# Performance work log

Measured on AMD Instinct MI355X. Metric: run time of the kernel, lower is better.

## Reference

```python
import jax, jax.numpy as jnp
import numpy as np

B, D_IN, D_OUT = 8192, 1024, 1024


def setup_inputs() -> dict:
    key = jax.random.key(0)
    k1, k2 = jax.random.split(key)
    x = jax.random.normal(k1, (B, D_IN), dtype=jnp.float32)
    # Keras add_weight(shape=(3, input_dim, output_dim), initializer='uniform')
    kernel = jax.random.normal(k2, (3, D_IN, D_OUT), dtype=jnp.float32) * 0.05
    return {"x": x, "kernel": kernel}


def reference(x, kernel):
    # x: (B, D). Layer does expand_dims(axis=1) -> (B, 1, D) (seq_len == 1).
    output_dim = kernel.shape[-1]
    xe = x[:, None, :]                                   # (B, 1, D)
    q = jnp.einsum('bsd,do->bso', xe, kernel[0])         # (B, 1, O)
    k = jnp.einsum('bsd,do->bso', xe, kernel[1])         # (B, 1, O)
    v = jnp.einsum('bsd,do->bso', xe, kernel[2])         # (B, 1, O)
    scores = jnp.einsum('bqo,bko->bqk', q, k) / jnp.sqrt(
        jnp.asarray(output_dim, x.dtype))                # (B, 1, 1)
    attn = jax.nn.softmax(scores, axis=-1)
    out = jnp.einsum('bqk,bko->bqo', attn, v)            # (B, 1, O)
    return out
```

## Files before the change

kernel.cpp:

```cpp
#include <hip/hip_runtime.h>
#include <hip/hip_bf16.h>
#include <stdint.h>

#define AS1 __attribute__((address_space(1)))
#define AS3 __attribute__((address_space(3)))

typedef __attribute__((ext_vector_type(8))) short bf16x8_t;
typedef __attribute__((ext_vector_type(4))) float f32x4_t;

#define DDIM 1024
#define BM 128
#define BN 128
#define BK 32

static __device__ inline ushort f32_to_bf16_rne(float f) {
  union { float f; uint32_t u; } v;
  v.f = f;
  v.u += 0x7FFFu + ((v.u >> 16) & 1u);
  return (ushort)(v.u >> 16);
}

__global__ __launch_bounds__(256) void transpose_w(const float* __restrict__ W,
                                                   ushort* __restrict__ Wt) {
  __shared__ float tile[64][65];
  const int t  = threadIdx.x;
  const int bk = blockIdx.x;
  const int bn = blockIdx.y;
#pragma unroll
  for (int s = 0; s < 4; ++s) {
    const int slot = (s << 8) + t;
    const int r    = slot >> 4;
    const int c4   = (slot & 15) << 2;
    const float4 v = *(const float4*)(W + (size_t)(bk * 64 + r) * DDIM + bn * 64 + c4);
    tile[r][c4 + 0] = v.x; tile[r][c4 + 1] = v.y;
    tile[r][c4 + 2] = v.z; tile[r][c4 + 3] = v.w;
  }
  __syncthreads();
#pragma unroll
  for (int s = 0; s < 2; ++s) {
    const int slot = (s << 8) + t;
    const int n    = slot >> 3;
    const int k8   = (slot & 7) << 3;
    union { ushort h[8]; uint4 u; } tmp;
#pragma unroll
    for (int j = 0; j < 8; ++j) tmp.h[j] = f32_to_bf16_rne(tile[k8 + j][n]);
    *(uint4*)(Wt + (size_t)(bn * 64 + n) * DDIM + bk * 64 + k8) = tmp.u;
  }
}

__global__ __launch_bounds__(256) void gemm_xw(const float* __restrict__ X,
                                               const ushort* __restrict__ Wt,
                                               float* __restrict__ C) {
  __shared__ __align__(16) ushort As[BM * BK];
  __shared__ __align__(16) ushort Bs[BN * BK];

  const int t    = threadIdx.x;
  const int wave = t >> 6;
  const int lane = t & 63;
  const int m0 = blockIdx.x * BM;
  const int n0 = blockIdx.y * BN;

  const int srow  = (wave << 4) + (lane >> 2);
  const int skcol = (lane & 3) << 3;
  const ushort* bptr0 = Wt + (size_t)(n0 + srow) * DDIM + skcol;
  const ushort* bptr1 = Wt + (size_t)(n0 + 64 + srow) * DDIM + skcol;

  const int ar = t >> 2;
  const int ak = (t & 3) << 3;
  const float* aptr0 = X + (size_t)(m0 + ar) * DDIM + ak;
  const float* aptr1 = X + (size_t)(m0 + 64 + ar) * DDIM + ak;
  ushort* asw0 = &As[(ar << 5) + ak];
  ushort* asw1 = &As[((ar + 64) << 5) + ak];

  const int wr = (wave >> 1) << 6;
  const int wc = (wave & 1) << 6;
  const int fr = lane & 15;
  const int fq = lane >> 4;

  f32x4_t acc[4][4] = {};

  AS3 char* ldsB = (AS3 char*)Bs;
  const int woff = wave << 10;

  for (int kt = 0; kt < DDIM; kt += BK) {
    const float4 a00 = *(const float4*)(aptr0);
    const float4 a01 = *(const float4*)(aptr0 + 4);
    const float4 a10 = *(const float4*)(aptr1);
    const float4 a11 = *(const float4*)(aptr1 + 4);
    aptr0 += BK; aptr1 += BK;

    __syncthreads();

    __builtin_amdgcn_global_load_lds((const AS1 void*)bptr0, (AS3 void*)(ldsB + woff),        16, 0, 0);
    __builtin_amdgcn_global_load_lds((const AS1 void*)bptr1, (AS3 void*)(ldsB + 4096 + woff), 16, 0, 0);
    bptr0 += BK; bptr1 += BK;

    union { ushort h[8]; bf16x8_t v; } c0, c1;
    c0.h[0] = f32_to_bf16_rne(a00.x); c0.h[1] = f32_to_bf16_rne(a00.y);
    c0.h[2] = f32_to_bf16_rne(a00.z); c0.h[3] = f32_to_bf16_rne(a00.w);
    c0.h[4] = f32_to_bf16_rne(a01.x); c0.h[5] = f32_to_bf16_rne(a01.y);
    c0.h[6] = f32_to_bf16_rne(a01.z); c0.h[7] = f32_to_bf16_rne(a01.w);
    c1.h[0] = f32_to_bf16_rne(a10.x); c1.h[1] = f32_to_bf16_rne(a10.y);
    c1.h[2] = f32_to_bf16_rne(a10.z); c1.h[3] = f32_to_bf16_rne(a10.w);
    c1.h[4] = f32_to_bf16_rne(a11.x); c1.h[5] = f32_to_bf16_rne(a11.y);
    c1.h[6] = f32_to_bf16_rne(a11.z); c1.h[7] = f32_to_bf16_rne(a11.w);
    *(bf16x8_t*)asw0 = c0.v;
    *(bf16x8_t*)asw1 = c1.v;

    __syncthreads();

    bf16x8_t af[4], bfr[4];
#pragma unroll
    for (int mi = 0; mi < 4; ++mi)
      af[mi] = *(const bf16x8_t*)&As[((wr + (mi << 4) + fr) << 5) + (fq << 3)];
#pragma unroll
    for (int ni = 0; ni < 4; ++ni)
      bfr[ni] = *(const bf16x8_t*)&Bs[((wc + (ni << 4) + fr) << 5) + (fq << 3)];
#pragma unroll
    for (int mi = 0; mi < 4; ++mi)
#pragma unroll
      for (int ni = 0; ni < 4; ++ni)
        acc[mi][ni] = __builtin_amdgcn_mfma_f32_16x16x32_bf16(af[mi], bfr[ni], acc[mi][ni], 0, 0, 0);
  }

#pragma unroll
  for (int mi = 0; mi < 4; ++mi) {
#pragma unroll
    for (int r = 0; r < 4; ++r) {
      const int row = m0 + wr + (mi << 4) + (fq << 2) + r;
      float* crow = C + (size_t)row * DDIM + n0 + wc + fr;
#pragma unroll
      for (int ni = 0; ni < 4; ++ni)
        crow[ni << 4] = acc[mi][ni][r];
    }
  }
}

extern "C" void kernel_launch(void* const* d_in, const int* in_sizes, int n_in,
                              void* d_out, int out_size, void* d_ws, size_t ws_size,
                              hipStream_t stream) {
  const float* x    = (const float*)d_in[0];
  const float* kern = (const float*)d_in[1];
  const float* W = kern + (size_t)2 * DDIM * DDIM;
  ushort* Wt = (ushort*)d_ws;
  const int M = in_sizes[0] / DDIM;

  transpose_w<<<dim3(DDIM / 64, DDIM / 64), 256, 0, stream>>>(W, Wt);
  gemm_xw<<<dim3(M / BM, DDIM / BN), 256, 0, stream>>>(x, Wt, (float*)d_out);
}
```

Before: 130.7 us.

## Pre-convert X to bf16 and use smaller-tile swizzled all-DMA GEMM

Adds a separate kernel that converts X to bf16 in workspace, then runs a new GEMM that loads both A and B tiles straight into LDS with global_load_lds. It uses a 64x128 tile with launch bounds for higher occupancy and an XOR swizzle to avoid LDS bank conflicts. This removes the per-iteration fp32 load and convert from the GEMM main loop. In exchange it adds an extra pass over X (read fp32, write bf16, reread) and one more launch, and falls back to the old path if the workspace is too small.

```diff
diff --git a/kernel.cpp b/kernel.cpp
--- a/kernel.cpp
+++ b/kernel.cpp
@@ -9,9 +9,8 @@
 typedef __attribute__((ext_vector_type(4))) float f32x4_t;
 
 #define DDIM 1024
-#define BM 128
-#define BN 128
-#define BK 32
+#define WT_ELEMS ((size_t)DDIM * DDIM)
+#define XB_ELEMS ((size_t)8192 * DDIM)
 
 static __device__ inline ushort f32_to_bf16_rne(float f) {
   union { float f; uint32_t u; } v;
@@ -48,53 +47,125 @@
   }
 }
 
+__global__ __launch_bounds__(256) void convert_x(const float* __restrict__ X,
+                                                 ushort* __restrict__ Xb) {
+  const size_t i = ((size_t)blockIdx.x * 256 + threadIdx.x) << 3;
+  const float4 v0 = *(const float4*)(X + i);
+  const float4 v1 = *(const float4*)(X + i + 4);
+  union { ushort h[8]; uint4 u; } o;
+  o.h[0] = f32_to_bf16_rne(v0.x); o.h[1] = f32_to_bf16_rne(v0.y);
+  o.h[2] = f32_to_bf16_rne(v0.z); o.h[3] = f32_to_bf16_rne(v0.w);
+  o.h[4] = f32_to_bf16_rne(v1.x); o.h[5] = f32_to_bf16_rne(v1.y);
+  o.h[6] = f32_to_bf16_rne(v1.z); o.h[7] = f32_to_bf16_rne(v1.w);
+  *(uint4*)(Xb + i) = o.u;
+}
+
+__global__ __launch_bounds__(256, 4) void gemm_bb(const ushort* __restrict__ Xb,
+                                                  const ushort* __restrict__ Wt,
+                                                  float* __restrict__ C) {
+  __shared__ __align__(16) ushort As[64 * 32];
+  __shared__ __align__(16) ushort Bs[128 * 32];
+
+  const int t    = threadIdx.x;
+  const int wave = t >> 6;
+  const int lane = t & 63;
+  const int m0 = blockIdx.x * 64;
+  const int n0 = blockIdx.y * 128;
+
+  const int s  = (wave << 6) + lane;
+  const int sr = s >> 2;
+  const int sc = (s & 3) ^ ((sr >> 1) & 3);
+  const ushort* aptr  = Xb + (size_t)(m0 + sr) * DDIM + (sc << 3);
+  const ushort* bptr0 = Wt + (size_t)(n0 + sr) * DDIM + (sc << 3);
+  const ushort* bptr1 = Wt + (size_t)(n0 + 64 + sr) * DDIM + (sc << 3);
+
+  AS3 char* ldsA = (AS3 char*)As;
+  AS3 char* ldsB = (AS3 char*)Bs;
+  const int woff = wave << 10;
+
+  const int wr = (wave >> 1) << 5;
+  const int wc = (wave & 1) << 6;
+  const int fr = lane & 15;
+  const int fq = lane >> 4;
+
+  f32x4_t acc[2][4] = {};
+
+  for (int kt = 0; kt < DDIM; kt += 32) {
+    __syncthreads();
+    __builtin_amdgcn_global_load_lds((const AS1 void*)aptr,  (AS3 void*)(ldsA + woff),        16, 0, 0);
+    __builtin_amdgcn_global_load_lds((const AS1 void*)bptr0, (AS3 void*)(ldsB + woff),        16, 0, 0);
+    __builtin_amdgcn_global_load_lds((const AS1 void*)bptr1, (AS3 void*)(ldsB + 4096 + woff), 16, 0, 0);
+    aptr += 32; bptr0 += 32; bptr1 += 32;
+    __syncthreads();
+
+    bf16x8_t af[2], bfr[4];
+#pragma unroll
+    for (int mi = 0; mi < 2; ++mi) {
+      const int r = wr + (mi << 4) + fr;
+      af[mi] = *(const bf16x8_t*)&As[(r << 5) + ((fq ^ ((r >> 1) & 3)) << 3)];
+    }
+#pragma unroll
+    for (int ni = 0; ni < 4; ++ni) {
+      const int r = wc + (ni << 4) + fr;
+      bfr[ni] = *(const bf16x8_t*)&Bs[(r << 5) + ((fq ^ ((r >> 1) & 3)) << 3)];
+    }
+#pragma unroll
+    for (int mi = 0; mi < 2; ++mi)
+#pragma unroll
+      for (int ni = 0; ni < 4; ++ni)
+        acc[mi][ni] = __builtin_amdgcn_mfma_f32_16x16x32_bf16(af[mi], bfr[ni], acc[mi][ni], 0, 0, 0);
+  }
+
+#pragma unroll
+  for (int mi = 0; mi < 2; ++mi) {
+#pragma unroll
+    for (int r = 0; r < 4; ++r) {
+      const int row = m0 + wr + (mi << 4) + (fq << 2) + r;
+      float* crow = C + (size_t)row * DDIM + n0 + wc + fr;
+#pragma unroll
+      for (int ni = 0; ni < 4; ++ni)
+        crow[ni << 4] = acc[mi][ni][r];
+    }
+  }
+}
+
 __global__ __launch_bounds__(256) void gemm_xw(const float* __restrict__ X,
                                                const ushort* __restrict__ Wt,
                                                float* __restrict__ C) {
-  __shared__ __align__(16) ushort As[BM * BK];
-  __shared__ __align__(16) ushort Bs[BN * BK];
-
+  __shared__ __align__(16) ushort As[128 * 32];
+  __shared__ __align__(16) ushort Bs[128 * 32];
   const int t    = threadIdx.x;
   const int wave = t >> 6;
   const int lane = t & 63;
-  const int m0 = blockIdx.x * BM;
-  const int n0 = blockIdx.y * BN;
-
+  const int m0 = blockIdx.x * 128;
+  const int n0 = blockIdx.y * 128;
   const int srow  = (wave << 4) + (lane >> 2);
   const int skcol = (lane & 3) << 3;
   const ushort* bptr0 = Wt + (size_t)(n0 + srow) * DDIM + skcol;
   const ushort* bptr1 = Wt + (size_t)(n0 + 64 + srow) * DDIM + skcol;
-
   const int ar = t >> 2;
   const int ak = (t & 3) << 3;
   const float* aptr0 = X + (size_t)(m0 + ar) * DDIM + ak;
   const float* aptr1 = X + (size_t)(m0 + 64 + ar) * DDIM + ak;
   ushort* asw0 = &As[(ar << 5) + ak];
   ushort* asw1 = &As[((ar + 64) << 5) + ak];
-
   const int wr = (wave >> 1) << 6;
   const int wc = (wave & 1) << 6;
   const int fr = lane & 15;
   const int fq = lane >> 4;
-
   f32x4_t acc[4][4] = {};
-
   AS3 char* ldsB = (AS3 char*)Bs;
   const int woff = wave << 10;
-
-  for (int kt = 0; kt < DDIM; kt += BK) {
+  for (int kt = 0; kt < DDIM; kt += 32) {
     const float4 a00 = *(const float4*)(aptr0);
     const float4 a01 = *(const float4*)(aptr0 + 4);
     const float4 a10 = *(const float4*)(aptr1);
     const float4 a11 = *(const float4*)(aptr1 + 4);
-    aptr0 += BK; aptr1 += BK;
-
-    __syncthreads();
-
+    aptr0 += 32; aptr1 += 32;
+    __syncthreads();
     __builtin_amdgcn_global_load_lds((const AS1 void*)bptr0, (AS3 void*)(ldsB + woff),        16, 0, 0);
     __builtin_amdgcn_global_load_lds((const AS1 void*)bptr1, (AS3 void*)(ldsB + 4096 + woff), 16, 0, 0);
-    bptr0 += BK; bptr1 += BK;
-
+    bptr0 += 32; bptr1 += 32;
     union { ushort h[8]; bf16x8_t v; } c0, c1;
     c0.h[0] = f32_to_bf16_rne(a00.x); c0.h[1] = f32_to_bf16_rne(a00.y);
     c0.h[2] = f32_to_bf16_rne(a00.z); c0.h[3] = f32_to_bf16_rne(a00.w);
@@ -106,9 +177,7 @@
     c1.h[6] = f32_to_bf16_rne(a11.z); c1.h[7] = f32_to_bf16_rne(a11.w);
     *(bf16x8_t*)asw0 = c0.v;
     *(bf16x8_t*)asw1 = c1.v;
-
-    __syncthreads();
-
+    __syncthreads();
     bf16x8_t af[4], bfr[4];
 #pragma unroll
     for (int mi = 0; mi < 4; ++mi)
@@ -122,9 +191,8 @@
       for (int ni = 0; ni < 4; ++ni)
         acc[mi][ni] = __builtin_amdgcn_mfma_f32_16x16x32_bf16(af[mi], bfr[ni], acc[mi][ni], 0, 0, 0);
   }
-
-#pragma unroll
-  for (int mi = 0; mi < 4; ++mi) {
+#pragma unroll
+  for (int mi = 0; mi < 4; ++mi)
 #pragma unroll
     for (int r = 0; r < 4; ++r) {
       const int row = m0 + wr + (mi << 4) + (fq << 2) + r;
@@ -133,7 +201,6 @@
       for (int ni = 0; ni < 4; ++ni)
         crow[ni << 4] = acc[mi][ni][r];
     }
-  }
 }
 
 extern "C" void kernel_launch(void* const* d_in, const int* in_sizes, int n_in,
@@ -146,5 +213,12 @@
   const int M = in_sizes[0] / DDIM;
 
   transpose_w<<<dim3(DDIM / 64, DDIM / 64), 256, 0, stream>>>(W, Wt);
-  gemm_xw<<<dim3(M / BM, DDIM / BN), 256, 0, stream>>>(x, Wt, (float*)d_out);
-}
+
+  if (ws_size >= (WT_ELEMS + XB_ELEMS) * sizeof(ushort)) {
+    ushort* Xb = (ushort*)d_ws + WT_ELEMS;
+    convert_x<<<(unsigned)((size_t)M * DDIM / 8 / 256), 256, 0, stream>>>(x, Xb);
+    gemm_bb<<<dim3(M / 64, DDIM / 128), 256, 0, stream>>>(Xb, Wt, (float*)d_out);
+  } else {
+    gemm_xw<<<dim3(M / 128, DDIM / 128), 256, 0, stream>>>(x, Wt, (float*)d_out);
+  }
+}
```

After: 117.8 us. 1.11x faster.
